# Optimization experiments

Measured on AMD Instinct MI355X. Metric: run time of the kernel, lower is better.

Reference implementation:

```python
import jax, jax.numpy as jnp
import numpy as np

INPUT_SIZE = 2048
HIDDEN_SIZE = 2048
BATCH = 4096
COMBINED = INPUT_SIZE + HIDDEN_SIZE


def setup_inputs() -> dict:
    key = jax.random.key(0)
    ks = jax.random.split(key, 11)
    s = 1.0 / np.sqrt(COMBINED)  # torch Linear default init scale
    inp = {
        "x_t": jax.random.normal(ks[0], (BATCH, INPUT_SIZE), jnp.float32),
        "h_prev": jax.random.normal(ks[1], (BATCH, HIDDEN_SIZE), jnp.float32),
        "c_prev": jax.random.normal(ks[2], (BATCH, HIDDEN_SIZE), jnp.float32),
        # torch nn.Linear weights: [out, in]
        "W_f": jax.random.uniform(ks[3], (HIDDEN_SIZE, COMBINED), jnp.float32, -s, s),
        "b_f": jax.random.uniform(ks[4], (HIDDEN_SIZE,), jnp.float32, -s, s),
        "W_i": jax.random.uniform(ks[5], (HIDDEN_SIZE, COMBINED), jnp.float32, -s, s),
        "b_i": jax.random.uniform(ks[6], (HIDDEN_SIZE,), jnp.float32, -s, s),
        "W_c": jax.random.uniform(ks[7], (HIDDEN_SIZE, COMBINED), jnp.float32, -s, s),
        "b_c": jax.random.uniform(ks[8], (HIDDEN_SIZE,), jnp.float32, -s, s),
        "W_o": jax.random.uniform(ks[9], (HIDDEN_SIZE, COMBINED), jnp.float32, -s, s),
        "b_o": jax.random.uniform(ks[10], (HIDDEN_SIZE,), jnp.float32, -s, s),
    }
    return inp


def reference(x_t, h_prev, c_prev, W_f, b_f, W_i, b_i, W_c, b_c, W_o, b_o):
    # combined = cat([h_prev, x_t], dim=1)  -> [B, H + I]
    combined = jnp.concatenate([h_prev, x_t], axis=1)
    # Fuse the four gate GEMMs into one [B, C] x [C, 4H] matmul.
    W = jnp.concatenate([W_f, W_i, W_c, W_o], axis=0)  # [4H, C]
    b = jnp.concatenate([b_f, b_i, b_c, b_o], axis=0)  # [4H]
    gates = combined @ W.T + b  # [B, 4H]
    gf, gi, gc, go = jnp.split(gates, 4, axis=1)
    f_t = jax.nn.sigmoid(gf)
    i_t = jax.nn.sigmoid(gi)
    c_tilde = jnp.tanh(gc)
    o_t = jax.nn.sigmoid(go)
    c_t = f_t * c_prev + i_t * c_tilde
    h_t = o_t * jnp.tanh(c_t)
    return (h_t, c_t)
```

## Files before the change

kernel.cpp:

```cpp
#include <hip/hip_runtime.h>
#include <hip/hip_bf16.h>
#include <cstdint>

#define B_DIM 4096
#define H_DIM 2048
#define I_DIM 2048
#define K_DIM 4096
#define N4    8192

typedef unsigned int u32;
typedef unsigned short u16;
typedef __attribute__((ext_vector_type(4))) float floatx4;
typedef __attribute__((ext_vector_type(8))) short bf16x8;
typedef __attribute__((ext_vector_type(8))) unsigned short ushort8_t;

__device__ static inline u16 f2bf(float f) {
    union { float f; u32 u; } v; v.f = f;
    u32 u = v.u;
    return (u16)((u + 0x7FFFu + ((u >> 16) & 1u)) >> 16);
}
__device__ static inline void gload16(const void* g, void* l) {
    __builtin_amdgcn_global_load_lds(
        (const __attribute__((address_space(1))) u32*)g,
        (__attribute__((address_space(3))) u32*)l, 16, 0, 0);
}
__device__ static inline float fast_sig(float x) {
    return 1.f / (1.f + __expf(-x));
}
__device__ static inline float fast_tanh(float x) {
    float ax = fabsf(x);
    float t = __expf(-2.f * ax);
    float r = (1.f - t) / (1.f + t);
    return copysignf(r, x);
}

__global__ void convert_all(const float* __restrict__ h_prev, const float* __restrict__ x_t,
                            const float* __restrict__ Wf, const float* __restrict__ Wi,
                            const float* __restrict__ Wc, const float* __restrict__ Wo,
                            u16* __restrict__ comb, u16* __restrict__ wb) {
    const int bid = blockIdx.x;
    const float* src;
    u16* dst;
    if (bid < 8192) {
        int base = (bid * 256 + (int)threadIdx.x) * 8;
        int row = base >> 12, col = base & 4095;
        src = (col < H_DIM) ? h_prev + (size_t)row * H_DIM + col
                            : x_t    + (size_t)row * I_DIM + (col - H_DIM);
        dst = comb + base;
    } else {
        long long base = ((long long)(bid - 8192) * 256 + threadIdx.x) * 8;
        int n = (int)(base >> 12), col = (int)(base & 4095);
        int row128 = n & 127;
        int g = (row128 >> 4) & 3;
        int j = (n >> 7) * 32 + ((row128 >> 6) << 4) + (row128 & 15);
        const float* W = (g == 0) ? Wf : (g == 1) ? Wi : (g == 2) ? Wc : Wo;
        src = W + (size_t)j * K_DIM + col;
        dst = wb + base;
    }
    float4 v0 = *(const float4*)src;
    float4 v1 = *(const float4*)(src + 4);
    ushort8_t o = { f2bf(v0.x), f2bf(v0.y), f2bf(v0.z), f2bf(v0.w),
                    f2bf(v1.x), f2bf(v1.y), f2bf(v1.z), f2bf(v1.w) };
    *(ushort8_t*)dst = o;
}

__global__ __launch_bounds__(256) void gemm_lstm(const u16* __restrict__ A,
                                                 const u16* __restrict__ Bm,
                                                 const float* __restrict__ c_prev,
                                                 const float* __restrict__ bf_,
                                                 const float* __restrict__ bi_,
                                                 const float* __restrict__ bc_,
                                                 const float* __restrict__ bo_,
                                                 float* __restrict__ out) {
    __shared__ u16 lsA[128 * 32];
    __shared__ u16 lsB[128 * 32];

    const int tid   = threadIdx.x;
    const int lane  = tid & 63;
    const int wave  = tid >> 6;
    const int wm    = (wave & 1) * 64;
    const int wpart = wave >> 1;
    const int wn    = wpart * 64;
    const int quad  = lane >> 4;
    const int r     = lane & 15;
    const int mb    = blockIdx.y * 128;
    const int nbT   = blockIdx.x * 128;

    floatx4 acc[4][4];
#pragma unroll
    for (int i = 0; i < 4; i++)
#pragma unroll
        for (int g = 0; g < 4; g++)
            acc[i][g] = (floatx4){0.f, 0.f, 0.f, 0.f};

    for (int kt = 0; kt < K_DIM; kt += 32) {
        __syncthreads();
#pragma unroll
        for (int s = 0; s < 2; s++) {
            int c   = tid + s * 256;
            int row = c >> 2;
            int ko  = (c & 3) * 8;
            gload16(A  + (size_t)(mb + row) * K_DIM + kt + ko, (char*)lsA + c * 16);
            gload16(Bm + (size_t)(nbT + row) * K_DIM + kt + ko, (char*)lsB + c * 16);
        }
        __syncthreads();

        bf16x8 af[4], bfr[4];
#pragma unroll
        for (int i = 0; i < 4; i++)
            af[i] = *(const bf16x8*)&lsA[(wm + i * 16 + r) * 32 + quad * 8];
#pragma unroll
        for (int g = 0; g < 4; g++)
            bfr[g] = *(const bf16x8*)&lsB[(wn + g * 16 + r) * 32 + quad * 8];
#pragma unroll
        for (int i = 0; i < 4; i++)
#pragma unroll
            for (int g = 0; g < 4; g++)
                acc[i][g] = __builtin_amdgcn_mfma_f32_16x16x32_bf16(
                    af[i], bfr[g], acc[i][g], 0, 0, 0);
    }

    __builtin_amdgcn_sched_barrier(0);

    const int j = blockIdx.x * 32 + wpart * 16 + r;
    const float bfv = bf_[j], biv = bi_[j], bcv = bc_[j], bov = bo_[j];
    const float* cp = c_prev + (size_t)(mb + wm + quad * 4) * H_DIM + j;
    float* oh = out + (size_t)(mb + wm + quad * 4) * H_DIM + j;
    float* oc = oh + (size_t)B_DIM * H_DIM;
#pragma unroll
    for (int i = 0; i < 4; i++) {
#pragma unroll
        for (int rg = 0; rg < 4; rg++) {
            size_t off = (size_t)(i * 16 + rg) * H_DIM;
            float gf = acc[i][0][rg] + bfv;
            float gi = acc[i][1][rg] + biv;
            float gc = acc[i][2][rg] + bcv;
            float go = acc[i][3][rg] + bov;
            float f  = fast_sig(gf);
            float ii = fast_sig(gi);
            float ct = fast_tanh(gc);
            float oo = fast_sig(go);
            float c = f * cp[off] + ii * ct;
            float h = oo * fast_tanh(c);
            oh[off] = h;
            oc[off] = c;
        }
    }
}

__global__ void lstm_naive(const float* __restrict__ x_t, const float* __restrict__ h_prev,
                           const float* __restrict__ c_prev,
                           const float* __restrict__ Wf, const float* __restrict__ bf_,
                           const float* __restrict__ Wi, const float* __restrict__ bi_,
                           const float* __restrict__ Wc, const float* __restrict__ bc_,
                           const float* __restrict__ Wo, const float* __restrict__ bo_,
                           float* __restrict__ out) {
    int j = blockIdx.x * blockDim.x + threadIdx.x;
    int b = blockIdx.y;
    const float* hrow = h_prev + (long long)b * H_DIM;
    const float* xrow = x_t   + (long long)b * I_DIM;
    const float* wf = Wf + (long long)j * K_DIM;
    const float* wi = Wi + (long long)j * K_DIM;
    const float* wc = Wc + (long long)j * K_DIM;
    const float* wo = Wo + (long long)j * K_DIM;
    float af = bf_[j], ai = bi_[j], ac = bc_[j], ao = bo_[j];
    for (int k = 0; k < H_DIM; k += 4) {
        float4 v = *(const float4*)(hrow + k);
        float4 a = *(const float4*)(wf + k);
        float4 bqi = *(const float4*)(wi + k);
        float4 cq = *(const float4*)(wc + k);
        float4 dq = *(const float4*)(wo + k);
        af += v.x*a.x + v.y*a.y + v.z*a.z + v.w*a.w;
        ai += v.x*bqi.x + v.y*bqi.y + v.z*bqi.z + v.w*bqi.w;
        ac += v.x*cq.x + v.y*cq.y + v.z*cq.z + v.w*cq.w;
        ao += v.x*dq.x + v.y*dq.y + v.z*dq.z + v.w*dq.w;
    }
    for (int k = 0; k < I_DIM; k += 4) {
        float4 v = *(const float4*)(xrow + k);
        float4 a = *(const float4*)(wf + H_DIM + k);
        float4 bqi = *(const float4*)(wi + H_DIM + k);
        float4 cq = *(const float4*)(wc + H_DIM + k);
        float4 dq = *(const float4*)(wo + H_DIM + k);
        af += v.x*a.x + v.y*a.y + v.z*a.z + v.w*a.w;
        ai += v.x*bqi.x + v.y*bqi.y + v.z*bqi.z + v.w*bqi.w;
        ac += v.x*cq.x + v.y*cq.y + v.z*cq.z + v.w*cq.w;
        ao += v.x*dq.x + v.y*dq.y + v.z*dq.z + v.w*dq.w;
    }
    float f  = 1.f / (1.f + __expf(-af));
    float ii = 1.f / (1.f + __expf(-ai));
    float ct = tanhf(ac);
    float oo = 1.f / (1.f + __expf(-ao));
    int t = b * H_DIM + j;
    float c = f * c_prev[t] + ii * ct;
    out[t] = oo * tanhf(c);
    out[B_DIM * H_DIM + t] = c;
}

extern "C" void kernel_launch(void* const* d_in, const int* in_sizes, int n_in,
                              void* d_out, int out_size, void* d_ws, size_t ws_size,
                              hipStream_t stream) {
    const float* x_t    = (const float*)d_in[0];
    const float* h_prev = (const float*)d_in[1];
    const float* c_prev = (const float*)d_in[2];
    const float* Wf = (const float*)d_in[3];  const float* bf_ = (const float*)d_in[4];
    const float* Wi = (const float*)d_in[5];  const float* bi_ = (const float*)d_in[6];
    const float* Wc = (const float*)d_in[7];  const float* bc_ = (const float*)d_in[8];
    const float* Wo = (const float*)d_in[9];  const float* bo_ = (const float*)d_in[10];
    float* out = (float*)d_out;

    const size_t comb_elems = (size_t)B_DIM * K_DIM;
    const size_t wb_elems   = (size_t)N4 * K_DIM;
    const size_t need = (comb_elems + wb_elems) * sizeof(u16);

    if (ws_size >= need) {
        u16* comb = (u16*)d_ws;
        u16* wb   = comb + comb_elems;
        convert_all<<<24576, 256, 0, stream>>>(h_prev, x_t, Wf, Wi, Wc, Wo, comb, wb);
        dim3 grid(N4 / 128, B_DIM / 128);
        gemm_lstm<<<grid, 256, 0, stream>>>(comb, wb, c_prev, bf_, bi_, bc_, bo_, out);
    } else {
        dim3 grid(H_DIM / 256, B_DIM);
        lstm_naive<<<grid, 256, 0, stream>>>(x_t, h_prev, c_prev,
                                             Wf, bf_, Wi, bi_, Wc, bc_, Wo, bo_, out);
    }
}
```

Measured before the change: 569.2 us.

## Double GEMM K-tile to 64 with XOR-swizzled LDS layout and nontemporal stores

```diff
diff --git a/kernel.cpp b/kernel.cpp
--- a/kernel.cpp
+++ b/kernel.cpp
@@ -7,6 +7,7 @@
 #define I_DIM 2048
 #define K_DIM 4096
 #define N4    8192
+#define BK    64
 
 typedef unsigned int u32;
 typedef unsigned short u16;
@@ -72,8 +73,8 @@
                                                  const float* __restrict__ bc_,
                                                  const float* __restrict__ bo_,
                                                  float* __restrict__ out) {
-    __shared__ u16 lsA[128 * 32];
-    __shared__ u16 lsB[128 * 32];
+    __shared__ u16 lsA[128 * BK];
+    __shared__ u16 lsB[128 * BK];
 
     const int tid   = threadIdx.x;
     const int lane  = tid & 63;
@@ -93,31 +94,41 @@
         for (int g = 0; g < 4; g++)
             acc[i][g] = (floatx4){0.f, 0.f, 0.f, 0.f};
 
-    for (int kt = 0; kt < K_DIM; kt += 32) {
+    for (int kt = 0; kt < K_DIM; kt += BK) {
         __syncthreads();
 #pragma unroll
-        for (int s = 0; s < 2; s++) {
-            int c   = tid + s * 256;
-            int row = c >> 2;
-            int ko  = (c & 3) * 8;
-            gload16(A  + (size_t)(mb + row) * K_DIM + kt + ko, (char*)lsA + c * 16);
-            gload16(Bm + (size_t)(nbT + row) * K_DIM + kt + ko, (char*)lsB + c * 16);
+        for (int s4 = 0; s4 < 4; s4++) {
+            int c    = tid + s4 * 256;
+            int row  = c >> 3;
+            int slot = c & 7;
+            int gch  = slot ^ (row & 7);
+            gload16(A  + (size_t)(mb + row) * K_DIM + kt + gch * 8, (char*)lsA + c * 16);
+            gload16(Bm + (size_t)(nbT + row) * K_DIM + kt + gch * 8, (char*)lsB + c * 16);
         }
         __syncthreads();
 
-        bf16x8 af[4], bfr[4];
-#pragma unroll
-        for (int i = 0; i < 4; i++)
-            af[i] = *(const bf16x8*)&lsA[(wm + i * 16 + r) * 32 + quad * 8];
-#pragma unroll
-        for (int g = 0; g < 4; g++)
-            bfr[g] = *(const bf16x8*)&lsB[(wn + g * 16 + r) * 32 + quad * 8];
-#pragma unroll
-        for (int i = 0; i < 4; i++)
-#pragma unroll
-            for (int g = 0; g < 4; g++)
-                acc[i][g] = __builtin_amdgcn_mfma_f32_16x16x32_bf16(
-                    af[i], bfr[g], acc[i][g], 0, 0, 0);
+#pragma unroll
+        for (int sub = 0; sub < 2; sub++) {
+            bf16x8 af[4], bfr[4];
+#pragma unroll
+            for (int i = 0; i < 4; i++) {
+                int row = wm + i * 16 + r;
+                int sl  = ((sub << 2) + quad) ^ (r & 7);
+                af[i] = *(const bf16x8*)&lsA[row * BK + sl * 8];
+            }
+#pragma unroll
+            for (int g = 0; g < 4; g++) {
+                int row = wn + g * 16 + r;
+                int sl  = ((sub << 2) + quad) ^ (r & 7);
+                bfr[g] = *(const bf16x8*)&lsB[row * BK + sl * 8];
+            }
+#pragma unroll
+            for (int i = 0; i < 4; i++)
+#pragma unroll
+                for (int g = 0; g < 4; g++)
+                    acc[i][g] = __builtin_amdgcn_mfma_f32_16x16x32_bf16(
+                        af[i], bfr[g], acc[i][g], 0, 0, 0);
+        }
     }
 
     __builtin_amdgcn_sched_barrier(0);
@@ -142,8 +153,8 @@
             float oo = fast_sig(go);
             float c = f * cp[off] + ii * ct;
             float h = oo * fast_tanh(c);
-            oh[off] = h;
-            oc[off] = c;
+            __builtin_nontemporal_store(h, &oh[off]);
+            __builtin_nontemporal_store(c, &oc[off]);
         }
     }
 }
```

After: 576.9 us. About the same (+1.4%).
